# Kernel optimization log

Measured on AMD Instinct MI355X. Metric: run time of the kernel, lower is better.

Reference implementation:

```python
import jax, jax.numpy as jnp
import numpy as np

B, S, D, H = 2, 2048, 1024, 16
HD = D // H

def setup_inputs() -> dict:
    key = jax.random.key(0)
    ks = jax.random.split(key, 9)
    scale = 1.0 / np.sqrt(D)
    return {
        "query": jax.random.normal(ks[0], (B, S, D), jnp.float32),
        "key":   jax.random.normal(ks[1], (B, S, D), jnp.float32),
        "value": jax.random.normal(ks[2], (B, S, D), jnp.float32),
        "Wq_w": jax.random.normal(ks[3], (D, D), jnp.float32) * scale,
        "Wq_b": jax.random.normal(ks[4], (D,), jnp.float32) * scale,
        "Wk_w": jax.random.normal(ks[5], (D, D), jnp.float32) * scale,
        "Wk_b": jax.random.normal(ks[6], (D,), jnp.float32) * scale,
        "Wv_w": jax.random.normal(ks[7], (D, D), jnp.float32) * scale,
        "Wv_b": jax.random.normal(ks[8], (D,), jnp.float32) * scale,
    }

def reference(query, key, value, Wq_w, Wq_b, Wk_w, Wk_b, Wv_w, Wv_b):
    b, s, d = query.shape
    # torch Linear: y = x @ W.T + b
    Q = query @ Wq_w.T + Wq_b
    K = key   @ Wk_w.T + Wk_b
    V = value @ Wv_w.T + Wv_b
    # [B, H, S, HD]
    Q = Q.reshape(b, -1, H, HD).transpose(0, 2, 1, 3)
    K = K.reshape(b, -1, H, HD).transpose(0, 2, 1, 3)
    V = V.reshape(b, -1, H, HD).transpose(0, 2, 1, 3)
    scores = jnp.einsum("bhqd,bhkd->bhqk", Q, K) / jnp.sqrt(jnp.float32(HD))
    attn = jax.nn.softmax(scores, axis=-1)
    context = jnp.einsum("bhqk,bhkd->bhqd", attn, V)  # [B,H,S,HD]
    attn_output = context.transpose(0, 2, 1, 3).reshape(b, -1, H * HD)  # [B,S,D]
    return (context, attn_output)
```

## Files before the change

### kernel.cpp

```cpp
#include <hip/hip_runtime.h>
#include <hip/hip_bf16.h>

constexpr int Bb = 2, Ss = 2048, Dd = 1024, Hh = 16, HD = 64;
constexpr int Mrows = Bb * Ss;
constexpr float QSCALE = 0.125f * 1.44269504088896f;
constexpr size_t CTX_ELEMS = (size_t)Bb * Hh * Ss * HD;

typedef __attribute__((ext_vector_type(8)))  short        short8;
typedef __attribute__((ext_vector_type(4)))  float        floatx4;
typedef __attribute__((ext_vector_type(16))) float        floatx16;
typedef __attribute__((ext_vector_type(4)))  unsigned int uintx4;
typedef __attribute__((ext_vector_type(8)))  __bf16       bf16x8;

#define DEVI __device__ __forceinline__

DEVI unsigned short f2bf(float f) {
  union { float f; unsigned u; } x; x.f = f;
  return (unsigned short)((x.u + 0x7fffu + ((x.u >> 16) & 1u)) >> 16);
}
DEVI float fexp2(float x) {
#if __has_builtin(__builtin_amdgcn_exp2f)
  return __builtin_amdgcn_exp2f(x);
#else
  return __expf(x * 0.6931471805599453f);
#endif
}

constexpr size_t XE = (size_t)Mrows * Dd;
constexpr size_t WE = (size_t)Dd * Dd;
constexpr size_t OFF_W = 3 * XE;
constexpr size_t OFF_O = 3 * XE + 3 * WE;
constexpr size_t WS_NEED = (OFF_O + 3 * XE) * 2;

__global__ __launch_bounds__(256) void convert_bf16(
    const float* __restrict__ q, const float* __restrict__ k, const float* __restrict__ v,
    const float* __restrict__ wq, const float* __restrict__ wk, const float* __restrict__ wv,
    unsigned short* __restrict__ dst)
{
  const int sel = blockIdx.y;
  const float* src; size_t n, off;
  switch (sel) {
    case 0:  src = q;  n = XE; off = 0;            break;
    case 1:  src = k;  n = XE; off = XE;           break;
    case 2:  src = v;  n = XE; off = 2 * XE;       break;
    case 3:  src = wq; n = WE; off = OFF_W;        break;
    case 4:  src = wk; n = WE; off = OFF_W + WE;   break;
    default: src = wv; n = WE; off = OFF_W + 2*WE; break;
  }
  unsigned short* d = dst + off;
  const size_t stride = (size_t)gridDim.x * blockDim.x;
  for (size_t i = (size_t)blockIdx.x * blockDim.x + threadIdx.x; i < n / 8; i += stride) {
    const floatx4 a = *(const floatx4*)(src + i * 8);
    const floatx4 b = *(const floatx4*)(src + i * 8 + 4);
    short8 o;
    #pragma unroll
    for (int j = 0; j < 4; ++j) { o[j] = (short)f2bf(a[j]); o[4 + j] = (short)f2bf(b[j]); }
    *(short8*)(d + i * 8) = o;
  }
}

template<bool SWAP>
DEVI void store_out(floatx4 (&acc)[4][4], const float* __restrict__ bias,
                    unsigned short* __restrict__ out, float oscale,
                    int bm, int bn, int wm, int wn, int lrow, int lg)
{
  if constexpr (!SWAP) {
    #pragma unroll
    for (int ni = 0; ni < 4; ++ni) {
      const int gcol = bn * 128 + wn + ni * 16 + lrow;
      const float bval = bias[gcol];
      const int h = gcol >> 6, hd = gcol & 63;
      #pragma unroll
      for (int mi = 0; mi < 4; ++mi)
        #pragma unroll
        for (int r = 0; r < 4; ++r) {
          const int grow = bm * 128 + wm + mi * 16 + lg * 4 + r;
          const int b = grow >> 11, s = grow & 2047;
          out[(((size_t)(b * Hh + h) * Ss + s) << 6) + hd] = f2bf((acc[mi][ni][r] + bval) * oscale);
        }
    }
  } else {
    #pragma unroll
    for (int ni = 0; ni < 4; ++ni)
      #pragma unroll
      for (int r = 0; r < 4; ++r) {
        const int n = bn * 128 + wn + ni * 16 + lg * 4 + r;
        const float bval = bias[n];
        #pragma unroll
        for (int mi = 0; mi < 4; ++mi) {
          const int m = bm * 128 + wm + mi * 16 + lrow;
          out[(size_t)n * Mrows + m] = f2bf(acc[mi][ni][r] + bval);
        }
      }
  }
}

DEVI void gload16(const unsigned short* g, unsigned short* l) {
  __builtin_amdgcn_global_load_lds(
      (const __attribute__((address_space(1))) unsigned int*)g,
      (__attribute__((address_space(3))) unsigned int*)l, 16, 0, 0);
}

template<bool SWAP>
DEVI void gemm_core_bf16(const unsigned short* __restrict__ X,
                         const unsigned short* __restrict__ W,
                         const float* __restrict__ bias,
                         unsigned short* __restrict__ out, float oscale,
                         unsigned short* As, unsigned short* Bs, int bm, int bn)
{
  const int t = threadIdx.x, wid = t >> 6, lane = t & 63;
  const int lrow = lane & 15, lg = lane >> 4;
  const int wm = (wid >> 1) * 64, wn = (wid & 1) * 64;

  const int srow = lane >> 3;
  const int gch  = (lane & 7) ^ srow;
  const unsigned short* gA = X + (size_t)(bm * 128 + wid * 32 + srow) * Dd + gch * 8;
  const unsigned short* gB = W + (size_t)(bn * 128 + wid * 32 + srow) * Dd + gch * 8;
  unsigned short* lA = As + wid * 4 * 512;
  unsigned short* lB = Bs + wid * 4 * 512;

  floatx4 acc[4][4];
  #pragma unroll
  for (int i = 0; i < 4; ++i)
    #pragma unroll
    for (int j = 0; j < 4; ++j) acc[i][j] = 0.0f;

  for (int k0 = 0; k0 < Dd; k0 += 64) {
    __syncthreads();
    #pragma unroll
    for (int j = 0; j < 4; ++j) {
      gload16(gA + (size_t)j * 8 * Dd + k0, lA + j * 512);
      gload16(gB + (size_t)j * 8 * Dd + k0, lB + j * 512);
    }
    __syncthreads();

    #pragma unroll
    for (int kf = 0; kf < 2; ++kf) {
      bf16x8 af[4], bf[4];
      #pragma unroll
      for (int mi = 0; mi < 4; ++mi) {
        const int row = wm + mi * 16 + lrow;
        const int ch  = ((kf << 2) | lg) ^ (lrow & 7);
        af[mi] = __builtin_bit_cast(bf16x8, *(const short8*)&As[row * 64 + (ch << 3)]);
      }
      #pragma unroll
      for (int ni = 0; ni < 4; ++ni) {
        const int row = wn + ni * 16 + lrow;
        const int ch  = ((kf << 2) | lg) ^ (lrow & 7);
        bf[ni] = __builtin_bit_cast(bf16x8, *(const short8*)&Bs[row * 64 + (ch << 3)]);
      }
      #pragma unroll
      for (int mi = 0; mi < 4; ++mi)
        #pragma unroll
        for (int ni = 0; ni < 4; ++ni) {
          if constexpr (SWAP)
            acc[mi][ni] = __builtin_amdgcn_mfma_f32_16x16x32_bf16(bf[ni], af[mi], acc[mi][ni], 0, 0, 0);
          else
            acc[mi][ni] = __builtin_amdgcn_mfma_f32_16x16x32_bf16(af[mi], bf[ni], acc[mi][ni], 0, 0, 0);
        }
    }
  }
  store_out<SWAP>(acc, bias, out, oscale, bm, bn, wm, wn, lrow, lg);
}

__global__ __launch_bounds__(256, 3) void qkv_gemm_bf16(
    const unsigned short* __restrict__ ws,
    const float* __restrict__ bq, const float* __restrict__ bk, const float* __restrict__ bv,
    unsigned short* __restrict__ outbase)
{
  __shared__ __align__(16) unsigned short As[128 * 64];
  __shared__ __align__(16) unsigned short Bs[128 * 64];

  const int id  = blockIdx.y * 256 + blockIdx.x;
  const int swz = (id & 7) * 96 + (id >> 3);
  const int sel = swz >> 8;
  const int bx  = swz & 255;
  const int bm = bx >> 3, bn = bx & 7;

  const unsigned short* X = ws + (size_t)sel * XE;
  const unsigned short* W = ws + OFF_W + (size_t)sel * WE;
  const float* bias = sel == 0 ? bq : sel == 1 ? bk : bv;
  unsigned short* out = outbase + (size_t)sel * XE;

  if (sel == 2) gemm_core_bf16<true >(X, W, bias, out, 1.0f,   As, Bs, bm, bn);
  else          gemm_core_bf16<false>(X, W, bias, out, sel == 0 ? QSCALE : 1.0f, As, Bs, bm, bn);
}

constexpr int APAD = 40;

template<bool SWAP>
DEVI void gemm_core_f32(const float* __restrict__ X, const float* __restrict__ W,
                        const float* __restrict__ bias, unsigned short* __restrict__ out,
                        float oscale, unsigned short* As, unsigned short* Bs, int bm, int bn)
{
  const int t = threadIdx.x, wid = t >> 6, lane = t & 63;
  const int lrow = lane & 15, lg = lane >> 4;
  const int wm = (wid >> 1) * 64, wn = (wid & 1) * 64;

  floatx4 acc[4][4];
  #pragma unroll
  for (int i = 0; i < 4; ++i)
    #pragma unroll
    for (int j = 0; j < 4; ++j) acc[i][j] = 0.0f;

  for (int k0 = 0; k0 < Dd; k0 += 32) {
    __syncthreads();
    #pragma unroll
    for (int half = 0; half < 2; ++half) {
      const int cidx = t + half * 256;
      const int r = cidx >> 2, c = cidx & 3;
      {
        const float* ga = X + (size_t)(bm * 128 + r) * Dd + k0 + c * 8;
        const floatx4 x0 = *(const floatx4*)ga;
        const floatx4 x1 = *(const floatx4*)(ga + 4);
        short8 va;
        #pragma unroll
        for (int j = 0; j < 4; ++j) { va[j] = (short)f2bf(x0[j]); va[4+j] = (short)f2bf(x1[j]); }
        *(short8*)&As[r * APAD + c * 8] = va;
      }
      {
        const float* gb = W + (size_t)(bn * 128 + r) * Dd + k0 + c * 8;
        const floatx4 x0 = *(const floatx4*)gb;
        const floatx4 x1 = *(const floatx4*)(gb + 4);
        short8 vb;
        #pragma unroll
        for (int j = 0; j < 4; ++j) { vb[j] = (short)f2bf(x0[j]); vb[4+j] = (short)f2bf(x1[j]); }
        *(short8*)&Bs[r * APAD + c * 8] = vb;
      }
    }
    __syncthreads();

    bf16x8 af[4], bf[4];
    #pragma unroll
    for (int mi = 0; mi < 4; ++mi)
      af[mi] = __builtin_bit_cast(bf16x8, *(const short8*)&As[(wm + mi * 16 + lrow) * APAD + lg * 8]);
    #pragma unroll
    for (int ni = 0; ni < 4; ++ni)
      bf[ni] = __builtin_bit_cast(bf16x8, *(const short8*)&Bs[(wn + ni * 16 + lrow) * APAD + lg * 8]);

    #pragma unroll
    for (int mi = 0; mi < 4; ++mi)
      #pragma unroll
      for (int ni = 0; ni < 4; ++ni) {
        if constexpr (SWAP)
          acc[mi][ni] = __builtin_amdgcn_mfma_f32_16x16x32_bf16(bf[ni], af[mi], acc[mi][ni], 0, 0, 0);
        else
          acc[mi][ni] = __builtin_amdgcn_mfma_f32_16x16x32_bf16(af[mi], bf[ni], acc[mi][ni], 0, 0, 0);
      }
  }
  store_out<SWAP>(acc, bias, out, oscale, bm, bn, wm, wn, lrow, lg);
}

__global__ __launch_bounds__(256, 2) void qkv_gemm_f32(
    const float* __restrict__ q, const float* __restrict__ k, const float* __restrict__ v,
    const float* __restrict__ wq, const float* __restrict__ wk, const float* __restrict__ wv,
    const float* __restrict__ bq, const float* __restrict__ bk, const float* __restrict__ bv,
    unsigned short* __restrict__ outbase)
{
  __shared__ __align__(16) unsigned short As[128 * APAD];
  __shared__ __align__(16) unsigned short Bs[128 * APAD];

  const int id  = blockIdx.y * 256 + blockIdx.x;
  const int swz = (id & 7) * 96 + (id >> 3);
  const int sel = swz >> 8;
  const int bx  = swz & 255;
  const int bm = bx >> 3, bn = bx & 7;

  const float* X = sel == 0 ? q : sel == 1 ? k : v;
  const float* W = sel == 0 ? wq : sel == 1 ? wk : wv;
  const float* bias = sel == 0 ? bq : sel == 1 ? bk : bv;
  unsigned short* out = outbase + (size_t)sel * XE;

  if (sel == 2) gemm_core_f32<true >(X, W, bias, out, 1.0f, As, Bs, bm, bn);
  else          gemm_core_f32<false>(X, W, bias, out, sel == 0 ? QSCALE : 1.0f, As, Bs, bm, bn);
}

__global__ __launch_bounds__(256, 2) void attn_fwd(
    const unsigned short* __restrict__ Qw, const unsigned short* __restrict__ Kw,
    const unsigned short* __restrict__ Vw, float* __restrict__ out)
{
  __shared__ __align__(16) unsigned short Ks[2][64 * 64];
  __shared__ __align__(16) unsigned short Vt[2][64 * 64];

  const int id  = blockIdx.y * 16 + blockIdx.x;
  const int swz = (id & 7) * 64 + (id >> 3);
  const int qb  = swz & 15, bh = swz >> 4;
  const int b   = bh >> 4, h = bh & 15;

  const int t = threadIdx.x, wid = t >> 6, lane = t & 63;
  const int l31 = lane & 31, hi = lane >> 5;
  const unsigned short* Qb = Qw + (size_t)bh * (Ss * HD);
  const unsigned short* Kb = Kw + (size_t)bh * (Ss * HD);
  const unsigned short* Vg = Vw + (size_t)(h * 64) * Mrows + b * Ss;
  const int q0 = qb * 128 + wid * 32;

  bf16x8 qf[4];
  #pragma unroll
  for (int hs = 0; hs < 4; ++hs)
    qf[hs] = __builtin_bit_cast(bf16x8,
        *(const short8*)(Qb + (size_t)(q0 + l31) * 64 + hs * 16 + hi * 8));

  floatx16 ctx[2], lsum;
  #pragma unroll
  for (int nb = 0; nb < 2; ++nb) ctx[nb] = 0.0f;
  lsum = 0.0f;

  short8 ones_s;
  #pragma unroll
  for (int j = 0; j < 8; ++j) ones_s[j] = (short)0x3F80;
  const bf16x8 ones = __builtin_bit_cast(bf16x8, ones_s);

  const int rl = lane >> 3;
  const int cs = (lane & 7) ^ rl;
  auto stage = [&](int kv0, int buf) {
    #pragma unroll
    for (int i = 0; i < 2; ++i) {
      const int row = wid * 16 + i * 8 + rl;
      gload16(Kb + (size_t)(kv0 + row) * 64 + cs * 8, &Ks[buf][(wid * 16 + i * 8) * 64]);
      gload16(Vg + (size_t)row * Mrows + kv0 + cs * 8, &Vt[buf][(wid * 16 + i * 8) * 64]);
    }
  };

  stage(0, 0);

  for (int it = 0; it < Ss / 64; ++it) {
    const int cur = it & 1;
    __syncthreads();
    if (it + 1 < Ss / 64) stage((it + 1) * 64, cur ^ 1);

    floatx16 s[2];
    s[0] = 0.0f; s[1] = 0.0f;
    __builtin_amdgcn_s_setprio(1);
    #pragma unroll
    for (int kvb = 0; kvb < 2; ++kvb)
      #pragma unroll
      for (int hs = 0; hs < 4; ++hs) {
        const int ch = ((hs << 1) | hi) ^ (l31 & 7);
        const bf16x8 kf = __builtin_bit_cast(bf16x8,
            *(const short8*)&Ks[cur][(kvb * 32 + l31) * 64 + (ch << 3)]);
        s[kvb] = __builtin_amdgcn_mfma_f32_32x32x16_bf16(kf, qf[hs], s[kvb], 0, 0, 0);
      }
    __builtin_amdgcn_s_setprio(0);

    #pragma unroll
    for (int kvb = 0; kvb < 2; ++kvb) {
      float p[16];
      #pragma unroll
      for (int r = 0; r < 16; ++r) p[r] = fexp2(s[kvb][r]);
      unsigned int c[8];
      #pragma unroll
      for (int i = 0; i < 8; ++i)
        asm("v_cvt_pk_bf16_f32 %0, %1, %2" : "=v"(c[i]) : "v"(p[2 * i]), "v"(p[2 * i + 1]));

      #pragma unroll
      for (int ks2 = 0; ks2 < 2; ++ks2) {
        unsigned int w0 = c[4 * ks2 + 0], w2 = c[4 * ks2 + 2];
        unsigned int w1 = c[4 * ks2 + 1], w3 = c[4 * ks2 + 3];
        asm("v_permlane32_swap_b32 %0, %1" : "+v"(w0), "+v"(w2));
        asm("v_permlane32_swap_b32 %0, %1" : "+v"(w1), "+v"(w3));
        uintx4 paw; paw[0] = w0; paw[1] = w1; paw[2] = w2; paw[3] = w3;
        const bf16x8 pa = __builtin_bit_cast(bf16x8, paw);

        const int ks = kvb * 2 + ks2;
        __builtin_amdgcn_s_setprio(1);
        lsum = __builtin_amdgcn_mfma_f32_32x32x16_bf16(pa, ones, lsum, 0, 0, 0);
        #pragma unroll
        for (int nb = 0; nb < 2; ++nb) {
          const int ch = ((ks << 1) | hi) ^ (l31 & 7);
          const bf16x8 vf = __builtin_bit_cast(bf16x8,
              *(const short8*)&Vt[cur][(nb * 32 + l31) * 64 + (ch << 3)]);
          ctx[nb] = __builtin_amdgcn_mfma_f32_32x32x16_bf16(pa, vf, ctx[nb], 0, 0, 0);
        }
        __builtin_amdgcn_s_setprio(0);
      }
    }
  }

  #pragma unroll
  for (int r = 0; r < 16; ++r) {
    const float inv = 1.0f / lsum[r];
    const int qrow = q0 + (r & 3) + 8 * (r >> 2) + 4 * hi;
    #pragma unroll
    for (int nb = 0; nb < 2; ++nb) {
      const int hd = nb * 32 + l31;
      const float val = ctx[nb][r] * inv;
      out[((size_t)bh * Ss + qrow) * 64 + hd] = val;
      out[CTX_ELEMS + (((size_t)(b * Ss + qrow)) << 10) + (h << 6) + hd] = val;
    }
  }
}

extern "C" void kernel_launch(void* const* d_in, const int* in_sizes, int n_in,
                              void* d_out, int out_size, void* d_ws, size_t ws_size,
                              hipStream_t stream) {
  const float* q  = (const float*)d_in[0];
  const float* k  = (const float*)d_in[1];
  const float* v  = (const float*)d_in[2];
  const float* wq = (const float*)d_in[3];
  const float* bq = (const float*)d_in[4];
  const float* wk = (const float*)d_in[5];
  const float* bk = (const float*)d_in[6];
  const float* wv = (const float*)d_in[7];
  const float* bv = (const float*)d_in[8];
  unsigned short* ws = (unsigned short*)d_ws;
  float* out = (float*)d_out;

  if (ws_size >= WS_NEED) {
    convert_bf16<<<dim3(256, 6), 256, 0, stream>>>(q, k, v, wq, wk, wv, ws);
    qkv_gemm_bf16<<<dim3(256, 3), 256, 0, stream>>>(ws, bq, bk, bv, ws + OFF_O);
    attn_fwd<<<dim3(16, 32), 256, 0, stream>>>(ws + OFF_O, ws + OFF_O + XE, ws + OFF_O + 2 * XE, out);
  } else {
    qkv_gemm_f32<<<dim3(256, 3), 256, 0, stream>>>(q, k, v, wq, wk, wv, bq, bk, bv, ws);
    attn_fwd<<<dim3(16, 32), 256, 0, stream>>>(ws, ws + XE, ws + 2 * XE, out);
  }
}
```

Before: 92.97 us.

## Fuse activation bf16 conversion into QKV GEMM and split attention KV across two wave groups

```diff
diff --git a/kernel.cpp b/kernel.cpp
--- a/kernel.cpp
+++ b/kernel.cpp
@@ -25,37 +25,31 @@
   return __expf(x * 0.6931471805599453f);
 #endif
 }
+DEVI unsigned int cvtpk(float lo, float hi) {
+  unsigned int r;
+  asm("v_cvt_pk_bf16_f32 %0, %1, %2" : "=v"(r) : "v"(lo), "v"(hi));
+  return r;
+}
 
 constexpr size_t XE = (size_t)Mrows * Dd;
 constexpr size_t WE = (size_t)Dd * Dd;
-constexpr size_t OFF_W = 3 * XE;
-constexpr size_t OFF_O = 3 * XE + 3 * WE;
-constexpr size_t WS_NEED = (OFF_O + 3 * XE) * 2;
-
-__global__ __launch_bounds__(256) void convert_bf16(
-    const float* __restrict__ q, const float* __restrict__ k, const float* __restrict__ v,
+constexpr size_t OFF_O = 3 * WE;
+
+__global__ __launch_bounds__(256) void convert_w(
     const float* __restrict__ wq, const float* __restrict__ wk, const float* __restrict__ wv,
     unsigned short* __restrict__ dst)
 {
   const int sel = blockIdx.y;
-  const float* src; size_t n, off;
-  switch (sel) {
-    case 0:  src = q;  n = XE; off = 0;            break;
-    case 1:  src = k;  n = XE; off = XE;           break;
-    case 2:  src = v;  n = XE; off = 2 * XE;       break;
-    case 3:  src = wq; n = WE; off = OFF_W;        break;
-    case 4:  src = wk; n = WE; off = OFF_W + WE;   break;
-    default: src = wv; n = WE; off = OFF_W + 2*WE; break;
-  }
-  unsigned short* d = dst + off;
+  const float* src = sel == 0 ? wq : sel == 1 ? wk : wv;
+  unsigned short* d = dst + (size_t)sel * WE;
   const size_t stride = (size_t)gridDim.x * blockDim.x;
-  for (size_t i = (size_t)blockIdx.x * blockDim.x + threadIdx.x; i < n / 8; i += stride) {
+  for (size_t i = (size_t)blockIdx.x * blockDim.x + threadIdx.x; i < WE / 8; i += stride) {
     const floatx4 a = *(const floatx4*)(src + i * 8);
     const floatx4 b = *(const floatx4*)(src + i * 8 + 4);
-    short8 o;
-    #pragma unroll
-    for (int j = 0; j < 4; ++j) { o[j] = (short)f2bf(a[j]); o[4 + j] = (short)f2bf(b[j]); }
-    *(short8*)(d + i * 8) = o;
+    uintx4 o;
+    o[0] = cvtpk(a[0], a[1]); o[1] = cvtpk(a[2], a[3]);
+    o[2] = cvtpk(b[0], b[1]); o[3] = cvtpk(b[2], b[3]);
+    *(uintx4*)(d + i * 8) = o;
   }
 }
 
@@ -102,22 +96,48 @@
 }
 
 template<bool SWAP>
-DEVI void gemm_core_bf16(const unsigned short* __restrict__ X,
-                         const unsigned short* __restrict__ W,
-                         const float* __restrict__ bias,
-                         unsigned short* __restrict__ out, float oscale,
-                         unsigned short* As, unsigned short* Bs, int bm, int bn)
+DEVI void gemm_core_mixed(const float* __restrict__ X,
+                          const unsigned short* __restrict__ W,
+                          const float* __restrict__ bias,
+                          unsigned short* __restrict__ out, float oscale,
+                          unsigned short* As, unsigned short* Bs, int bm, int bn)
 {
   const int t = threadIdx.x, wid = t >> 6, lane = t & 63;
   const int lrow = lane & 15, lg = lane >> 4;
   const int wm = (wid >> 1) * 64, wn = (wid & 1) * 64;
 
+  const int ar = t >> 2;
+  const int acb = (t & 3) * 16;
+  const float* gAbase = X + (size_t)(bm * 128 + ar) * Dd + acb;
+
   const int srow = lane >> 3;
   const int gch  = (lane & 7) ^ srow;
-  const unsigned short* gA = X + (size_t)(bm * 128 + wid * 32 + srow) * Dd + gch * 8;
   const unsigned short* gB = W + (size_t)(bn * 128 + wid * 32 + srow) * Dd + gch * 8;
-  unsigned short* lA = As + wid * 4 * 512;
   unsigned short* lB = Bs + wid * 4 * 512;
+
+  floatx4 ra[2][4];
+  auto loadA = [&](int k0) {
+    #pragma unroll
+    for (int i = 0; i < 2; ++i)
+      #pragma unroll
+      for (int j = 0; j < 4; ++j)
+        ra[i][j] = *(const floatx4*)(gAbase + (size_t)i * 64 * Dd + k0 + j * 4);
+  };
+  auto writeA = [&]() {
+    #pragma unroll
+    for (int i = 0; i < 2; ++i) {
+      const int row = ar + i * 64;
+      #pragma unroll
+      for (int j2 = 0; j2 < 2; ++j2) {
+        const floatx4 a = ra[i][2 * j2], b = ra[i][2 * j2 + 1];
+        uintx4 w;
+        w[0] = cvtpk(a[0], a[1]); w[1] = cvtpk(a[2], a[3]);
+        w[2] = cvtpk(b[0], b[1]); w[3] = cvtpk(b[2], b[3]);
+        const int cc = (acb >> 3) + j2;
+        *(uintx4*)&As[row * 64 + ((cc ^ (row & 7)) << 3)] = w;
+      }
+    }
+  };
 
   floatx4 acc[4][4];
   #pragma unroll
@@ -125,14 +145,16 @@
     #pragma unroll
     for (int j = 0; j < 4; ++j) acc[i][j] = 0.0f;
 
+  loadA(0);
+
   for (int k0 = 0; k0 < Dd; k0 += 64) {
     __syncthreads();
-    #pragma unroll
-    for (int j = 0; j < 4; ++j) {
-      gload16(gA + (size_t)j * 8 * Dd + k0, lA + j * 512);
+    writeA();
+    #pragma unroll
+    for (int j = 0; j < 4; ++j)
       gload16(gB + (size_t)j * 8 * Dd + k0, lB + j * 512);
-    }
     __syncthreads();
+    if (k0 + 64 < Dd) loadA(k0 + 64);
 
     #pragma unroll
     for (int kf = 0; kf < 2; ++kf) {
@@ -163,8 +185,9 @@
   store_out<SWAP>(acc, bias, out, oscale, bm, bn, wm, wn, lrow, lg);
 }
 
-__global__ __launch_bounds__(256, 3) void qkv_gemm_bf16(
-    const unsigned short* __restrict__ ws,
+__global__ __launch_bounds__(256, 3) void qkv_gemm(
+    const float* __restrict__ q, const float* __restrict__ k, const float* __restrict__ v,
+    const unsigned short* __restrict__ wbf,
     const float* __restrict__ bq, const float* __restrict__ bk, const float* __restrict__ bv,
     unsigned short* __restrict__ outbase)
 {
@@ -177,118 +200,34 @@
   const int bx  = swz & 255;
   const int bm = bx >> 3, bn = bx & 7;
 
-  const unsigned short* X = ws + (size_t)sel * XE;
-  const unsigned short* W = ws + OFF_W + (size_t)sel * WE;
+  const float* X = sel == 0 ? q : sel == 1 ? k : v;
+  const unsigned short* W = wbf + (size_t)sel * WE;
   const float* bias = sel == 0 ? bq : sel == 1 ? bk : bv;
   unsigned short* out = outbase + (size_t)sel * XE;
 
-  if (sel == 2) gemm_core_bf16<true >(X, W, bias, out, 1.0f,   As, Bs, bm, bn);
-  else          gemm_core_bf16<false>(X, W, bias, out, sel == 0 ? QSCALE : 1.0f, As, Bs, bm, bn);
-}
-
-constexpr int APAD = 40;
-
-template<bool SWAP>
-DEVI void gemm_core_f32(const float* __restrict__ X, const float* __restrict__ W,
-                        const float* __restrict__ bias, unsigned short* __restrict__ out,
-                        float oscale, unsigned short* As, unsigned short* Bs, int bm, int bn)
-{
-  const int t = threadIdx.x, wid = t >> 6, lane = t & 63;
-  const int lrow = lane & 15, lg = lane >> 4;
-  const int wm = (wid >> 1) * 64, wn = (wid & 1) * 64;
-
-  floatx4 acc[4][4];
-  #pragma unroll
-  for (int i = 0; i < 4; ++i)
-    #pragma unroll
-    for (int j = 0; j < 4; ++j) acc[i][j] = 0.0f;
-
-  for (int k0 = 0; k0 < Dd; k0 += 32) {
-    __syncthreads();
-    #pragma unroll
-    for (int half = 0; half < 2; ++half) {
-      const int cidx = t + half * 256;
-      const int r = cidx >> 2, c = cidx & 3;
-      {
-        const float* ga = X + (size_t)(bm * 128 + r) * Dd + k0 + c * 8;
-        const floatx4 x0 = *(const floatx4*)ga;
-        const floatx4 x1 = *(const floatx4*)(ga + 4);
-        short8 va;
-        #pragma unroll
-        for (int j = 0; j < 4; ++j) { va[j] = (short)f2bf(x0[j]); va[4+j] = (short)f2bf(x1[j]); }
-        *(short8*)&As[r * APAD + c * 8] = va;
-      }
-      {
-        const float* gb = W + (size_t)(bn * 128 + r) * Dd + k0 + c * 8;
-        const floatx4 x0 = *(const floatx4*)gb;
-        const floatx4 x1 = *(const floatx4*)(gb + 4);
-        short8 vb;
-        #pragma unroll
-        for (int j = 0; j < 4; ++j) { vb[j] = (short)f2bf(x0[j]); vb[4+j] = (short)f2bf(x1[j]); }
-        *(short8*)&Bs[r * APAD + c * 8] = vb;
-      }
-    }
-    __syncthreads();
-
-    bf16x8 af[4], bf[4];
-    #pragma unroll
-    for (int mi = 0; mi < 4; ++mi)
-      af[mi] = __builtin_bit_cast(bf16x8, *(const short8*)&As[(wm + mi * 16 + lrow) * APAD + lg * 8]);
-    #pragma unroll
-    for (int ni = 0; ni < 4; ++ni)
-      bf[ni] = __builtin_bit_cast(bf16x8, *(const short8*)&Bs[(wn + ni * 16 + lrow) * APAD + lg * 8]);
-
-    #pragma unroll
-    for (int mi = 0; mi < 4; ++mi)
-      #pragma unroll
-      for (int ni = 0; ni < 4; ++ni) {
-        if constexpr (SWAP)
-          acc[mi][ni] = __builtin_amdgcn_mfma_f32_16x16x32_bf16(bf[ni], af[mi], acc[mi][ni], 0, 0, 0);
-        else
-          acc[mi][ni] = __builtin_amdgcn_mfma_f32_16x16x32_bf16(af[mi], bf[ni], acc[mi][ni], 0, 0, 0);
-      }
-  }
-  store_out<SWAP>(acc, bias, out, oscale, bm, bn, wm, wn, lrow, lg);
-}
-
-__global__ __launch_bounds__(256, 2) void qkv_gemm_f32(
-    const float* __restrict__ q, const float* __restrict__ k, const float* __restrict__ v,
-    const float* __restrict__ wq, const float* __restrict__ wk, const float* __restrict__ wv,
-    const float* __restrict__ bq, const float* __restrict__ bk, const float* __restrict__ bv,
-    unsigned short* __restrict__ outbase)
-{
-  __shared__ __align__(16) unsigned short As[128 * APAD];
-  __shared__ __align__(16) unsigned short Bs[128 * APAD];
-
-  const int id  = blockIdx.y * 256 + blockIdx.x;
-  const int swz = (id & 7) * 96 + (id >> 3);
-  const int sel = swz >> 8;
-  const int bx  = swz & 255;
-  const int bm = bx >> 3, bn = bx & 7;
-
-  const float* X = sel == 0 ? q : sel == 1 ? k : v;
-  const float* W = sel == 0 ? wq : sel == 1 ? wk : wv;
-  const float* bias = sel == 0 ? bq : sel == 1 ? bk : bv;
-  unsigned short* out = outbase + (size_t)sel * XE;
-
-  if (sel == 2) gemm_core_f32<true >(X, W, bias, out, 1.0f, As, Bs, bm, bn);
-  else          gemm_core_f32<false>(X, W, bias, out, sel == 0 ? QSCALE : 1.0f, As, Bs, bm, bn);
-}
-
-__global__ __launch_bounds__(256, 2) void attn_fwd(
+  if (sel == 2) gemm_core_mixed<true >(X, W, bias, out, 1.0f, As, Bs, bm, bn);
+  else          gemm_core_mixed<false>(X, W, bias, out, sel == 0 ? QSCALE : 1.0f, As, Bs, bm, bn);
+}
+
+__global__ __launch_bounds__(512, 4) void attn_fwd8(
     const unsigned short* __restrict__ Qw, const unsigned short* __restrict__ Kw,
     const unsigned short* __restrict__ Vw, float* __restrict__ out)
 {
-  __shared__ __align__(16) unsigned short Ks[2][64 * 64];
-  __shared__ __align__(16) unsigned short Vt[2][64 * 64];
+  __shared__ __align__(16) char smemRaw[65536];
+  unsigned short* KsB = (unsigned short*)smemRaw;
+  unsigned short* VtB = (unsigned short*)(smemRaw + 32768);
+  float* ctxL  = (float*)smemRaw;
+  float* lsumL = (float*)(smemRaw + 32768);
 
   const int id  = blockIdx.y * 16 + blockIdx.x;
   const int swz = (id & 7) * 64 + (id >> 3);
   const int qb  = swz & 15, bh = swz >> 4;
   const int b   = bh >> 4, h = bh & 15;
 
-  const int t = threadIdx.x, wid = t >> 6, lane = t & 63;
+  const int t = threadIdx.x, wid8 = t >> 6, lane = t & 63;
+  const int kh = wid8 >> 2, wid = wid8 & 3;
   const int l31 = lane & 31, hi = lane >> 5;
+  const int kvbase = kh << 10;
   const unsigned short* Qb = Qw + (size_t)bh * (Ss * HD);
   const unsigned short* Kb = Kw + (size_t)bh * (Ss * HD);
   const unsigned short* Vg = Vw + (size_t)(h * 64) * Mrows + b * Ss;
@@ -300,53 +239,49 @@
     qf[hs] = __builtin_bit_cast(bf16x8,
         *(const short8*)(Qb + (size_t)(q0 + l31) * 64 + hs * 16 + hi * 8));
 
-  floatx16 ctx[2], lsum;
-  #pragma unroll
-  for (int nb = 0; nb < 2; ++nb) ctx[nb] = 0.0f;
-  lsum = 0.0f;
-
-  short8 ones_s;
-  #pragma unroll
-  for (int j = 0; j < 8; ++j) ones_s[j] = (short)0x3F80;
-  const bf16x8 ones = __builtin_bit_cast(bf16x8, ones_s);
+  floatx16 ctx[2];
+  ctx[0] = 0.0f; ctx[1] = 0.0f;
+  float lsumv = 0.0f;
 
   const int rl = lane >> 3;
   const int cs = (lane & 7) ^ rl;
-  auto stage = [&](int kv0, int buf) {
+  auto stage = [&](int T) {
+    const int kv0 = kvbase + T * 64;
+    unsigned short* Kd = KsB + (size_t)(kh * 2 + (T & 1)) * 4096;
+    unsigned short* Vd = VtB + (size_t)(kh * 2 + (T & 1)) * 4096;
     #pragma unroll
     for (int i = 0; i < 2; ++i) {
       const int row = wid * 16 + i * 8 + rl;
-      gload16(Kb + (size_t)(kv0 + row) * 64 + cs * 8, &Ks[buf][(wid * 16 + i * 8) * 64]);
-      gload16(Vg + (size_t)row * Mrows + kv0 + cs * 8, &Vt[buf][(wid * 16 + i * 8) * 64]);
+      gload16(Kb + (size_t)(kv0 + row) * 64 + cs * 8, Kd + (wid * 16 + i * 8) * 64);
+      gload16(Vg + (size_t)row * Mrows + kv0 + cs * 8, Vd + (wid * 16 + i * 8) * 64);
     }
   };
 
-  stage(0, 0);
-
-  for (int it = 0; it < Ss / 64; ++it) {
+  stage(0);
+
+  for (int it = 0; it < 16; ++it) {
     const int cur = it & 1;
     __syncthreads();
-    if (it + 1 < Ss / 64) stage((it + 1) * 64, cur ^ 1);
-
-    floatx16 s[2];
-    s[0] = 0.0f; s[1] = 0.0f;
-    __builtin_amdgcn_s_setprio(1);
-    #pragma unroll
-    for (int kvb = 0; kvb < 2; ++kvb)
+    if (it + 1 < 16) stage(it + 1);
+    const unsigned short* Kc = KsB + (size_t)(kh * 2 + cur) * 4096;
+    const unsigned short* Vc = VtB + (size_t)(kh * 2 + cur) * 4096;
+
+    #pragma unroll
+    for (int kvb = 0; kvb < 2; ++kvb) {
+      floatx16 s = 0.0f;
+      __builtin_amdgcn_s_setprio(1);
       #pragma unroll
       for (int hs = 0; hs < 4; ++hs) {
         const int ch = ((hs << 1) | hi) ^ (l31 & 7);
         const bf16x8 kf = __builtin_bit_cast(bf16x8,
-            *(const short8*)&Ks[cur][(kvb * 32 + l31) * 64 + (ch << 3)]);
-        s[kvb] = __builtin_amdgcn_mfma_f32_32x32x16_bf16(kf, qf[hs], s[kvb], 0, 0, 0);
-      }
-    __builtin_amdgcn_s_setprio(0);
-
-    #pragma unroll
-    for (int kvb = 0; kvb < 2; ++kvb) {
+            *(const short8*)&Kc[(kvb * 32 + l31) * 64 + (ch << 3)]);
+        s = __builtin_amdgcn_mfma_f32_32x32x16_bf16(kf, qf[hs], s, 0, 0, 0);
+      }
+      __builtin_amdgcn_s_setprio(0);
+
       float p[16];
       #pragma unroll
-      for (int r = 0; r < 16; ++r) p[r] = fexp2(s[kvb][r]);
+      for (int r = 0; r < 16; ++r) { p[r] = fexp2(s[r]); lsumv += p[r]; }
       unsigned int c[8];
       #pragma unroll
       for (int i = 0; i < 8; ++i)
@@ -363,12 +298,11 @@
 
         const int ks = kvb * 2 + ks2;
         __builtin_amdgcn_s_setprio(1);
-        lsum = __builtin_amdgcn_mfma_f32_32x32x16_bf16(pa, ones, lsum, 0, 0, 0);
         #pragma unroll
         for (int nb = 0; nb < 2; ++nb) {
           const int ch = ((ks << 1) | hi) ^ (l31 & 7);
           const bf16x8 vf = __builtin_bit_cast(bf16x8,
-              *(const short8*)&Vt[cur][(nb * 32 + l31) * 64 + (ch << 3)]);
+              *(const short8*)&Vc[(nb * 32 + l31) * 64 + (ch << 3)]);
           ctx[nb] = __builtin_amdgcn_mfma_f32_32x32x16_bf16(pa, vf, ctx[nb], 0, 0, 0);
         }
         __builtin_amdgcn_s_setprio(0);
@@ -376,16 +310,34 @@
     }
   }
 
-  #pragma unroll
-  for (int r = 0; r < 16; ++r) {
-    const float inv = 1.0f / lsum[r];
-    const int qrow = q0 + (r & 3) + 8 * (r >> 2) + 4 * hi;
-    #pragma unroll
-    for (int nb = 0; nb < 2; ++nb) {
-      const int hd = nb * 32 + l31;
-      const float val = ctx[nb][r] * inv;
-      out[((size_t)bh * Ss + qrow) * 64 + hd] = val;
-      out[CTX_ELEMS + (((size_t)(b * Ss + qrow)) << 10) + (h << 6) + hd] = val;
+  float sa = lsumv, sb = lsumv;
+  asm("v_permlane32_swap_b32 %0, %1" : "+v"(sa), "+v"(sb));
+  const float tot = lsumv + (hi ? sa : sb);
+
+  __syncthreads();
+  if (kh == 1) {
+    #pragma unroll
+    for (int r = 0; r < 16; ++r)
+      #pragma unroll
+      for (int nb = 0; nb < 2; ++nb)
+        ctxL[(nb * 16 + r) * 256 + wid * 64 + lane] = ctx[nb][r];
+    if (hi == 0) lsumL[wid * 32 + l31] = tot;
+  }
+  __syncthreads();
+  if (kh == 0) {
+    if (hi == 0) lsumL[128 + wid * 32 + l31] = tot + lsumL[wid * 32 + l31];
+    #pragma unroll
+    for (int r = 0; r < 16; ++r) {
+      const int wr = (r & 3) + 8 * (r >> 2) + 4 * hi;
+      const float inv = 1.0f / lsumL[128 + wid * 32 + wr];
+      const int qrow = q0 + wr;
+      #pragma unroll
+      for (int nb = 0; nb < 2; ++nb) {
+        const int hd = nb * 32 + l31;
+        const float val = (ctx[nb][r] + ctxL[(nb * 16 + r) * 256 + wid * 64 + lane]) * inv;
+        out[((size_t)bh * Ss + qrow) * 64 + hd] = val;
+        out[CTX_ELEMS + (((size_t)(b * Ss + qrow)) << 10) + (h << 6) + hd] = val;
+      }
     }
   }
 }
@@ -405,12 +357,10 @@
   unsigned short* ws = (unsigned short*)d_ws;
   float* out = (float*)d_out;
 
-  if (ws_size >= WS_NEED) {
-    convert_bf16<<<dim3(256, 6), 256, 0, stream>>>(q, k, v, wq, wk, wv, ws);
-    qkv_gemm_bf16<<<dim3(256, 3), 256, 0, stream>>>(ws, bq, bk, bv, ws + OFF_O);
-    attn_fwd<<<dim3(16, 32), 256, 0, stream>>>(ws + OFF_O, ws + OFF_O + XE, ws + OFF_O + 2 * XE, out);
-  } else {
-    qkv_gemm_f32<<<dim3(256, 3), 256, 0, stream>>>(q, k, v, wq, wk, wv, bq, bk, bv, ws);
-    attn_fwd<<<dim3(16, 32), 256, 0, stream>>>(ws, ws + XE, ws + 2 * XE, out);
-  }
-}
+  unsigned short* wsW = ws;
+  unsigned short* wsO = ws + OFF_O;
+
+  convert_w<<<dim3(64, 3), 256, 0, stream>>>(wq, wk, wv, wsW);
+  qkv_gemm<<<dim3(256, 3), 256, 0, stream>>>(q, k, v, wsW, bq, bk, bv, wsO);
+  attn_fwd8<<<dim3(16, 32), 512, 0, stream>>>(wsO, wsO + XE, wsO + 2 * XE, out);
+}
```

Measured after the change: 89.76 us. -3.4%, faster.
